# Optimization experiments

Measured on AMD Instinct MI355X. Metric: run time of the kernel, lower is better.

Reference implementation:

```python
import jax, jax.numpy as jnp
import numpy as np

D_EMBED = 64
N_HEADS = 4
D_HEAD = D_EMBED // N_HEADS
D_FF = 96          # int(1.5 * d_embed)
D_MODEL = 128      # repeat_factor = d_model // d_embed = 2
EPS = 1e-5
B = 4
# (idx_start, kernel_size, channels_in, kernel_no) per layer of the source CNN
LAYERS = [(0, 9, 8, 256), (18688, 9, 16, 256), (55808, 9, 16, 512)]
N_PARAMS = 130048
MAX_SEQ = max(ks * cin for _, ks, cin, _ in LAYERS) + 1  # 145


def _kernel_indices(start, ks, cin, kno):
    # Static ragged slice indices: per kernel, its weights plus trailing bias.
    L = ks * cin
    base = start + np.arange(kno)[:, None] * L + np.arange(L)[None, :]
    bias = start + kno * L + np.arange(kno)
    return np.concatenate([base, bias[:, None]], axis=1)  # (kno, L+1)


_IDX = [jnp.asarray(_kernel_indices(*l)) for l in LAYERS]


def setup_inputs():
    key = jax.random.key(0)
    k = jax.random.split(key, 8)
    s = 1.0 / np.sqrt(D_EMBED)
    return {
        "x": jax.random.normal(k[0], (B, N_PARAMS), dtype=jnp.float32),
        "pos_emb": jax.random.normal(k[1], (MAX_SEQ, D_EMBED), dtype=jnp.float32) * s,
        "comp_token": jax.random.normal(k[2], (D_EMBED,), dtype=jnp.float32),
        "in_proj_w": jax.random.normal(k[3], (3 * D_EMBED, D_EMBED), dtype=jnp.float32) * s,
        "in_proj_b": jnp.zeros((3 * D_EMBED,), jnp.float32),
        "out_proj_w": jax.random.normal(k[4], (D_EMBED, D_EMBED), dtype=jnp.float32) * s,
        "out_proj_b": jnp.zeros((D_EMBED,), jnp.float32),
        "lin1_w": jax.random.normal(k[5], (D_FF, D_EMBED), dtype=jnp.float32) * s,
        "lin1_b": jnp.zeros((D_FF,), jnp.float32),
        "lin2_w": jax.random.normal(k[6], (D_EMBED, D_FF), dtype=jnp.float32) / np.sqrt(D_FF),
        "lin2_b": jnp.zeros((D_EMBED,), jnp.float32),
        "ln1_w": jnp.ones((D_EMBED,), jnp.float32),
        "ln1_b": jnp.zeros((D_EMBED,), jnp.float32),
        "ln2_w": jnp.ones((D_EMBED,), jnp.float32),
        "ln2_b": jnp.zeros((D_EMBED,), jnp.float32),
    }


def _layernorm(x, w, b):
    mu = jnp.mean(x, axis=-1, keepdims=True)
    var = jnp.mean(jnp.square(x - mu), axis=-1, keepdims=True)
    return (x - mu) * jax.lax.rsqrt(var + EPS) * w + b


def _encoder(t, in_proj_w, in_proj_b, out_proj_w, out_proj_b,
             lin1_w, lin1_b, lin2_w, lin2_b, ln1_w, ln1_b, ln2_w, ln2_b):
    # Post-norm TransformerEncoderLayer (relu, eval mode -> dropout = identity).
    M, S, _ = t.shape
    qkv = t @ in_proj_w.T + in_proj_b                     # (M, S, 3D)
    q, k, v = jnp.split(qkv, 3, axis=-1)
    heads = lambda u: u.reshape(M, S, N_HEADS, D_HEAD).transpose(0, 2, 1, 3)
    q, k, v = heads(q), heads(k), heads(v)
    attn = jax.nn.softmax(jnp.einsum('mhsd,mhtd->mhst', q, k) / np.sqrt(D_HEAD))
    o = jnp.einsum('mhst,mhtd->mhsd', attn, v).transpose(0, 2, 1, 3).reshape(M, S, D_EMBED)
    o = o @ out_proj_w.T + out_proj_b
    h = _layernorm(t + o, ln1_w, ln1_b)
    ff = jax.nn.relu(h @ lin1_w.T + lin1_b) @ lin2_w.T + lin2_b
    return _layernorm(h + ff, ln2_w, ln2_b)


def reference(x, pos_emb, comp_token, in_proj_w, in_proj_b, out_proj_w, out_proj_b,
              lin1_w, lin1_b, lin2_w, lin2_b, ln1_w, ln1_b, ln2_w, ln2_b):
    enc = (in_proj_w, in_proj_b, out_proj_w, out_proj_b,
           lin1_w, lin1_b, lin2_w, lin2_b, ln1_w, ln1_b, ln2_w, ln2_b)
    outs = []
    for idx in _IDX:  # fixed small loop over layers; kernels within a layer are batched
        K, n = idx.shape
        w = x[:, idx]                                     # (B, K, n) ragged gather
        tok = w[..., None] + pos_emb[:n]                  # scalar -> d_embed broadcast + pos add
        cls = jnp.broadcast_to(comp_token, (B, K, 1, D_EMBED))
        tok = jnp.concatenate([cls, tok], axis=2).reshape(B * K, n + 1, D_EMBED)
        y = _encoder(tok, *enc)[:, 0, :]                  # comp-token readout
        outs.append(y.reshape(B, K, D_EMBED))
    y = jnp.concatenate(outs, axis=1)                     # (B, 1024, d_embed)
    return jnp.tile(y, (1, 1, D_MODEL // D_EMBED))        # (B, 1024, d_model)
```

## Files before the change

kernel.cpp:

```cpp
#include <hip/hip_runtime.h>
#include <math.h>

#define NPAR 130048
#define EPSF 1e-5f

typedef _Float16 hfp;
typedef _Float16 h2x __attribute__((ext_vector_type(2)));
typedef _Float16 h4x __attribute__((ext_vector_type(4)));
typedef float    f4x __attribute__((ext_vector_type(4)));

#define BSTR  164
#define VSTR2 172
#define ATSTR 172
#define WOSTR 76
#define L2STRH 108

#define L_W    0
#define L_WB   2304
#define L_ATT  2320
#define L_INVS 7824
#define L_O    7888
#define L_H1   8496
#define L_R    9104
#define L_PRE  9968
#define L_VPOS 11056
#define L_BETA 16560
#define L_QK   17216
#define L_SM   17344
#define SM_Q0   0
#define SM_KCLS 64
#define SM_VCLS 128
#define SM_UK   192
#define SM_UV   256
#define SM_ALPH 320
#define SM_GAM  324
#define SM_QB   328
#define LDS_FLOATS 17676

template<int C>
__device__ __forceinline__ float dppf(float x) {
    return __int_as_float(__builtin_amdgcn_update_dpp(0, __float_as_int(x), C, 0xf, 0xf, false));
}
__device__ __forceinline__ float rowsum16(float x) {
    x += dppf<0x128>(x); x += dppf<0x124>(x); x += dppf<0x122>(x); x += dppf<0x121>(x);
    return x;
}
__device__ __forceinline__ unsigned packh2(float a, float b) {
    union { h2x h; unsigned u; } cv;
    cv.h.x = (hfp)a; cv.h.y = (hfp)b;
    return cv.u;
}
__device__ __forceinline__ h4x cvt4(f4x v) {
    h4x r; r.x = (hfp)v.x; r.y = (hfp)v.y; r.z = (hfp)v.z; r.w = (hfp)v.w; return r;
}

template<int L>
__device__ __forceinline__ void run_group(
    const float* __restrict__ x,  const float* __restrict__ pe,
    const float* __restrict__ ct, const float* __restrict__ W,
    const float* __restrict__ bq, const float* __restrict__ Wo,
    const float* __restrict__ bo, const float* __restrict__ L1w,
    const float* __restrict__ b1, const float* __restrict__ L2w,
    const float* __restrict__ b2,
    const float* __restrict__ ln1w, const float* __restrict__ ln1b,
    const float* __restrict__ ln2w, const float* __restrict__ ln2b,
    float* __restrict__ lds, float* __restrict__ out,
    int b, int k0, int start, int kno, int kgo)
{
    const int tid  = threadIdx.x;
    const int wave = tid >> 6;
    const int lane = tid & 63;
    const int e16  = lane & 15;
    const int g4   = (lane >> 4) * 4;
    const int c0   = e16 * 4;
    const hfp* ldsh = (const hfp*)lds;

    {
        const f4x* src = (const f4x*)(x + (size_t)b*NPAR + start + (size_t)k0*L);
        f4x* dst = (f4x*)(lds + L_W);
        #pragma unroll
        for (int c = 0; c < (4*L + 255)/256; ++c) {
            int i4 = c*256 + tid;
            if (i4 < 4*L) dst[i4] = src[i4];
        }
        if (tid < 16) lds[L_WB + tid] = x[(size_t)b*NPAR + start + (size_t)kno*L + k0 + tid];
    }
    if (tid < 192) {
        const f4x* wr4 = (const f4x*)(W + tid*64);
        const f4x* ct4 = (const f4x*)ct;
        float dotc = bq[tid], rsum = 0.f;
        #pragma unroll
        for (int e = 0; e < 16; ++e) {
            f4x wv = wr4[e], cc = ct4[e];
            dotc += (wv.x*cc.x + wv.y*cc.y) + (wv.z*cc.z + wv.w*cc.w);
            rsum += (wv.x + wv.y) + (wv.z + wv.w);
        }
        const int cls = tid >> 6, o = tid & 63;
        if (cls == 0)      lds[L_SM + SM_Q0 + o] = dotc;
        else if (cls == 1) { lds[L_SM + SM_KCLS + o] = dotc; lds[L_SM + SM_UK + o] = rsum; }
        else               { lds[L_SM + SM_VCLS + o] = dotc; lds[L_SM + SM_UV + o] = rsum; }
    }

    h4x wof[4];
    #pragma unroll
    for (int kt = 0; kt < 4; ++kt)
        wof[kt] = cvt4(*(const f4x*)(Wo + (16*wave + e16)*64 + kt*16 + g4));
    h4x l1f[2][4];
    float b1v[2];
    #pragma unroll
    for (int u = 0; u < 2; ++u) {
        const int tt = wave + 4*u;
        if (tt < 6) {
            #pragma unroll
            for (int kt = 0; kt < 4; ++kt)
                l1f[u][kt] = cvt4(*(const f4x*)(L1w + (16*tt + e16)*64 + kt*16 + g4));
            b1v[u] = b1[16*tt + e16];
        }
    }
    h4x l2f[6];
    #pragma unroll
    for (int kt = 0; kt < 6; ++kt)
        l2f[kt] = cvt4(*(const f4x*)(L2w + (16*wave + e16)*96 + kt*16 + g4));
    const int nw = 16*wave + e16;
    const float boct = bo[nw] + ct[nw];
    const float b2v  = b2[nw];
    const f4x ln1w4 = *(const f4x*)(ln1w + c0);
    const f4x ln1b4 = *(const f4x*)(ln1b + c0);
    const f4x ln2w4 = *(const f4x*)(ln2w + c0);
    const f4x ln2b4 = *(const f4x*)(ln2b + c0);
    __syncthreads();

    {
        const int h = wave, d = lane;
        float acc = 0.f;
        #pragma unroll
        for (int e = 0; e < 16; ++e)
            acc += lds[L_SM + SM_Q0 + h*16 + e] * W[(64 + h*16 + e)*64 + d];
        ((hfp*)(lds + L_QK))[h*64 + d] = (hfp)acc;
    }
    if (lane < 16) {
        const int h = wave, e = lane;
        const float q0e = lds[L_SM + SM_Q0 + h*16 + e];
        float pa = q0e * lds[L_SM + SM_UK + h*16 + e];
        float pg = q0e * lds[L_SM + SM_KCLS + h*16 + e];
        float pq = q0e * bq[64 + h*16 + e];
        pa = rowsum16(pa); pg = rowsum16(pg); pq = rowsum16(pq);
        if (e == 0) {
            lds[L_SM + SM_ALPH + h] = pa;
            lds[L_SM + SM_GAM  + h] = pg;
            lds[L_SM + SM_QB   + h] = pq;
        }
    }
    __syncthreads();

    {
        const int w = wave, r16 = lane & 15, kg = lane >> 4;
        h4x av[4];
        #pragma unroll
        for (int kt = 0; kt < 4; ++kt)
            av[kt] = cvt4(*(const f4x*)(W + (128 + 16*w + r16)*64 + kt*16 + kg*4));
        h4x ab[4];
        #pragma unroll
        for (int kt = 0; kt < 4; ++kt) {
            if (r16 < 4) ab[kt] = *(const h4x*)((const hfp*)(lds + L_QK) + r16*64 + kt*16 + kg*4);
            else         { h4x z; z.x = (hfp)0.f; z.y = (hfp)0.f; z.z = (hfp)0.f; z.w = (hfp)0.f; ab[kt] = z; }
        }
        const f4x bv4 = *(const f4x*)(bq + 128 + 16*w + kg*4);
        hfp* vpos_h = (hfp*)(lds + L_VPOS);
        #pragma unroll
        for (int jt = 0; jt < 10; ++jt) {
            const int j = jt*16 + r16;
            h4x bf[4];
            #pragma unroll
            for (int kt = 0; kt < 4; ++kt) {
                if (j < 145) bf[kt] = cvt4(*(const f4x*)(pe + j*64 + kt*16 + kg*4));
                else { h4x z; z.x = (hfp)0.f; z.y = (hfp)0.f; z.z = (hfp)0.f; z.w = (hfp)0.f; bf[kt] = z; }
            }
            f4x acc = (f4x){0.f,0.f,0.f,0.f};
            #pragma unroll
            for (int kt = 0; kt < 4; ++kt)
                acc = __builtin_amdgcn_mfma_f32_16x16x16f16(av[kt], bf[kt], acc, 0, 0, 0);
            #pragma unroll
            for (int rr = 0; rr < 4; ++rr) {
                if (j < 145) vpos_h[(16*w + kg*4 + rr)*VSTR2 + j] = (hfp)(acc[rr] + bv4[rr]);
            }
            if ((jt & 3) == w) {
                f4x accb = (f4x){0.f,0.f,0.f,0.f};
                #pragma unroll
                for (int kt = 0; kt < 4; ++kt)
                    accb = __builtin_amdgcn_mfma_f32_16x16x16f16(ab[kt], bf[kt], accb, 0, 0, 0);
                if (lane < 16) {
                    const int jj = jt*16 + lane;
                    if (jj < 145) {
                        #pragma unroll
                        for (int rr = 0; rr < 4; ++rr)
                            lds[L_BETA + rr*BSTR + jj] = accb[rr] + lds[L_SM + SM_QB + rr];
                    }
                }
            }
        }
    }
    if (tid < 64) {
        hfp* vpos_h = (hfp*)(lds + L_VPOS);
        const int d = tid;
        #pragma unroll
        for (int c = 145; c < 156; ++c) vpos_h[d*VSTR2 + c] = (hfp)0.f;
        vpos_h[d*VSTR2 + 156] = (hfp)lds[L_SM + SM_VCLS + d];
        vpos_h[d*VSTR2 + 157] = (hfp)lds[L_SM + SM_UV + d];
        vpos_h[d*VSTR2 + 158] = (hfp)0.f;
        vpos_h[d*VSTR2 + 159] = (hfp)0.f;
    }
    __syncthreads();

    {
        const int r = tid >> 2;
        const int m = r >> 2, h = r & 3, q = tid & 3;
        const float alpha = lds[L_SM + SM_ALPH + h];
        const float gam   = lds[L_SM + SM_GAM  + h];
        const float* wr = lds + L_W + m*L;
        const float* br = lds + L_BETA + h*BSTR;
        const float wbias = lds[L_WB + m];

        float mx = 0.25f * gam;
        #pragma unroll
        for (int t = 0; t < 10; ++t) {
            const int j0 = 16*t + 4*q;
            if (j0 + 3 < L) {
                f4x wv = *(const f4x*)(wr + j0);
                f4x bv = *(const f4x*)(br + j0);
                mx = fmaxf(mx, fmaf(alpha, wv.x, bv.x)*0.25f);
                mx = fmaxf(mx, fmaf(alpha, wv.y, bv.y)*0.25f);
                mx = fmaxf(mx, fmaf(alpha, wv.z, bv.z)*0.25f);
                mx = fmaxf(mx, fmaf(alpha, wv.w, bv.w)*0.25f);
            } else if (j0 <= L) {
                #pragma unroll
                for (int ee = 0; ee < 4; ++ee) {
                    int j = j0 + ee;
                    if (j <= L) {
                        float w = (j < L) ? wr[j] : wbias;
                        mx = fmaxf(mx, fmaf(alpha, w, br[j])*0.25f);
                    }
                }
            }
        }
        mx = fmaxf(mx, __shfl_xor(mx, 1));
        mx = fmaxf(mx, __shfl_xor(mx, 2));
        const float M = mx;

        unsigned* arow32 = (unsigned*)(lds + L_ATT) + r*(ATSTR/2);
        float S = 0.f, WS = 0.f;
        #pragma unroll
        for (int t = 0; t < 10; ++t) {
            const int j0 = 16*t + 4*q;
            if (j0 + 3 < L) {
                f4x wv = *(const f4x*)(wr + j0);
                f4x bv = *(const f4x*)(br + j0);
                float p0 = __expf(fmaf(alpha, wv.x, bv.x)*0.25f - M);
                float p1 = __expf(fmaf(alpha, wv.y, bv.y)*0.25f - M);
                float p2 = __expf(fmaf(alpha, wv.z, bv.z)*0.25f - M);
                float p3 = __expf(fmaf(alpha, wv.w, bv.w)*0.25f - M);
                S  += (p0 + p1) + (p2 + p3);
                WS += (p0*wv.x + p1*wv.y) + (p2*wv.z + p3*wv.w);
                uint2 u; u.x = packh2(p0, p1); u.y = packh2(p2, p3);
                *(uint2*)(arow32 + (j0 >> 1)) = u;
            } else if (j0 <= L) {
                float pv4[4] = {0.f, 0.f, 0.f, 0.f};
                #pragma unroll
                for (int ee = 0; ee < 4; ++ee) {
                    int j = j0 + ee;
                    if (j <= L) {
                        float w = (j < L) ? wr[j] : wbias;
                        float p = __expf(fmaf(alpha, w, br[j])*0.25f - M);
                        S += p; WS += p*w; pv4[ee] = p;
                    }
                }
                uint2 u; u.x = packh2(pv4[0], pv4[1]); u.y = packh2(pv4[2], pv4[3]);
                *(uint2*)(arow32 + (j0 >> 1)) = u;
            } else if (j0 != 156) {
                uint2 z; z.x = 0u; z.y = 0u;
                *(uint2*)(arow32 + (j0 >> 1)) = z;
            }
        }
        S  += __shfl_xor(S, 1);  S  += __shfl_xor(S, 2);
        WS += __shfl_xor(WS, 1); WS += __shfl_xor(WS, 2);
        const float pc = __expf(0.25f*gam - M);
        S += pc;
        if (q == 0) {
            lds[L_INVS + r] = 1.f / S;
            arow32[78] = packh2(pc, WS);
            arow32[79] = 0u;
        }
    }
    __syncthreads();

    {
        const hfp* atth = ldsh + L_ATT*2;
        const hfp* vpos_h = ldsh + L_VPOS*2;
        const int hh = wave;
        f4x vacc = (f4x){0.f,0.f,0.f,0.f};
        #pragma unroll
        for (int kt = 0; kt < 10; ++kt) {
            h4x a  = *(const h4x*)(atth + (e16*4 + hh)*ATSTR + kt*16 + g4);
            h4x bf = *(const h4x*)(vpos_h + (16*hh + e16)*VSTR2 + kt*16 + g4);
            vacc = __builtin_amdgcn_mfma_f32_16x16x16f16(a, bf, vacc, 0, 0, 0);
        }
        hfp* Oh = (hfp*)(lds + L_O);
        #pragma unroll
        for (int rr = 0; rr < 4; ++rr) {
            float sc = lds[L_INVS + (g4 + rr)*4 + hh];
            Oh[(g4 + rr)*WOSTR + 16*hh + e16] = (hfp)(vacc[rr] * sc);
        }
    }
    __syncthreads();

    {
        const hfp* Oh = ldsh + L_O*2;
        f4x pacc = (f4x){0.f,0.f,0.f,0.f};
        #pragma unroll
        for (int kt = 0; kt < 4; ++kt) {
            h4x a = *(const h4x*)(Oh + e16*WOSTR + kt*16 + g4);
            pacc = __builtin_amdgcn_mfma_f32_16x16x16f16(a, wof[kt], pacc, 0, 0, 0);
        }
        #pragma unroll
        for (int rr = 0; rr < 4; ++rr)
            lds[L_PRE + (g4 + rr)*68 + nw] = pacc[rr] + boct;
    }
    __syncthreads();

    {
        const int m = wave*4 + (lane >> 4);
        f4x pv = *(const f4x*)(lds + L_PRE + m*68 + c0);
        float s = (pv.x + pv.y) + (pv.z + pv.w);
        float mu = rowsum16(s) * (1.f/64.f);
        f4x d; d.x = pv.x-mu; d.y = pv.y-mu; d.z = pv.z-mu; d.w = pv.w-mu;
        float v = (d.x*d.x + d.y*d.y) + (d.z*d.z + d.w*d.w);
        float rs = rsqrtf(rowsum16(v)*(1.f/64.f) + EPSF);
        h4x hv;
        hv.x = (hfp)(d.x*rs*ln1w4.x + ln1b4.x);
        hv.y = (hfp)(d.y*rs*ln1w4.y + ln1b4.y);
        hv.z = (hfp)(d.z*rs*ln1w4.z + ln1b4.z);
        hv.w = (hfp)(d.w*rs*ln1w4.w + ln1b4.w);
        *(h4x*)((hfp*)(lds + L_H1) + m*WOSTR + c0) = hv;
    }
    __syncthreads();

    {
        const hfp* H1h = ldsh + L_H1*2;
        h4x af[4];
        #pragma unroll
        for (int kt = 0; kt < 4; ++kt) af[kt] = *(const h4x*)(H1h + e16*WOSTR + kt*16 + g4);
        hfp* Rh = (hfp*)(lds + L_R);
        #pragma unroll
        for (int u = 0; u < 2; ++u) {
            const int tt = wave + 4*u;
            if (tt < 6) {
                f4x racc = (f4x){0.f,0.f,0.f,0.f};
                #pragma unroll
                for (int kt = 0; kt < 4; ++kt)
                    racc = __builtin_amdgcn_mfma_f32_16x16x16f16(af[kt], l1f[u][kt], racc, 0, 0, 0);
                const int n = 16*tt + e16;
                #pragma unroll
                for (int rr = 0; rr < 4; ++rr)
                    Rh[(g4 + rr)*L2STRH + n] = (hfp)fmaxf(racc[rr] + b1v[u], 0.f);
            }
        }
    }
    __syncthreads();

    {
        const hfp* Rh2 = ldsh + L_R*2;
        f4x yacc = (f4x){0.f,0.f,0.f,0.f};
        #pragma unroll
        for (int kt = 0; kt < 6; ++kt) {
            h4x a = *(const h4x*)(Rh2 + e16*L2STRH + kt*16 + g4);
            yacc = __builtin_amdgcn_mfma_f32_16x16x16f16(a, l2f[kt], yacc, 0, 0, 0);
        }
        #pragma unroll
        for (int rr = 0; rr < 4; ++rr)
            lds[L_PRE + (g4 + rr)*68 + nw] = yacc[rr] + b2v;
    }
    __syncthreads();

    {
        const int m = wave*4 + (lane >> 4);
        f4x pv = *(const f4x*)(lds + L_PRE + m*68 + c0);
        h4x h1p = *(const h4x*)((const hfp*)(lds + L_H1) + m*WOSTR + c0);
        f4x tot;
        tot.x = pv.x + (float)h1p.x;
        tot.y = pv.y + (float)h1p.y;
        tot.z = pv.z + (float)h1p.z;
        tot.w = pv.w + (float)h1p.w;
        float s = (tot.x + tot.y) + (tot.z + tot.w);
        float mu = rowsum16(s) * (1.f/64.f);
        f4x d; d.x = tot.x-mu; d.y = tot.y-mu; d.z = tot.z-mu; d.w = tot.w-mu;
        float v = (d.x*d.x + d.y*d.y) + (d.z*d.z + d.w*d.w);
        float rs = rsqrtf(rowsum16(v)*(1.f/64.f) + EPSF);
        f4x y;
        y.x = d.x*rs*ln2w4.x + ln2b4.x;
        y.y = d.y*rs*ln2w4.y + ln2b4.y;
        y.z = d.z*rs*ln2w4.z + ln2b4.z;
        y.w = d.w*rs*ln2w4.w + ln2b4.w;
        float* ob = out + ((size_t)b*1024 + kgo + k0 + m)*128;
        *(f4x*)(ob + c0)      = y;
        *(f4x*)(ob + 64 + c0) = y;
    }
}

__global__ __launch_bounds__(256, 1) void k_all(
    const float* __restrict__ x,  const float* __restrict__ pe,
    const float* __restrict__ ct, const float* __restrict__ W,
    const float* __restrict__ bq, const float* __restrict__ Wo,
    const float* __restrict__ bo, const float* __restrict__ L1w,
    const float* __restrict__ b1, const float* __restrict__ L2w,
    const float* __restrict__ b2,
    const float* __restrict__ ln1w, const float* __restrict__ ln1b,
    const float* __restrict__ ln2w, const float* __restrict__ ln2b,
    float* __restrict__ out)
{
    __shared__ __align__(16) float lds[LDS_FLOATS];
    const int w = blockIdx.x;
    if (w < 64) {
        run_group<72>(x, pe, ct, W, bq, Wo, bo, L1w, b1, L2w, b2,
                      ln1w, ln1b, ln2w, ln2b, lds, out,
                      w >> 4, (w & 15)*16, 0, 256, 0);
    } else if (w < 128) {
        const int g = w - 64;
        run_group<144>(x, pe, ct, W, bq, Wo, bo, L1w, b1, L2w, b2,
                       ln1w, ln1b, ln2w, ln2b, lds, out,
                       g >> 4, (g & 15)*16, 18688, 256, 256);
    } else {
        const int g = w - 128;
        run_group<144>(x, pe, ct, W, bq, Wo, bo, L1w, b1, L2w, b2,
                       ln1w, ln1b, ln2w, ln2b, lds, out,
                       g >> 5, (g & 31)*16, 55808, 512, 512);
    }
}

extern "C" void kernel_launch(void* const* d_in, const int* in_sizes, int n_in,
                              void* d_out, int out_size, void* d_ws, size_t ws_size,
                              hipStream_t stream) {
    const float* x    = (const float*)d_in[0];
    const float* pe   = (const float*)d_in[1];
    const float* ct   = (const float*)d_in[2];
    const float* Wq   = (const float*)d_in[3];
    const float* bq   = (const float*)d_in[4];
    const float* Wo   = (const float*)d_in[5];
    const float* bo   = (const float*)d_in[6];
    const float* L1w  = (const float*)d_in[7];
    const float* b1   = (const float*)d_in[8];
    const float* L2w  = (const float*)d_in[9];
    const float* b2   = (const float*)d_in[10];
    const float* ln1w = (const float*)d_in[11];
    const float* ln1b = (const float*)d_in[12];
    const float* ln2w = (const float*)d_in[13];
    const float* ln2b = (const float*)d_in[14];
    float* out = (float*)d_out;

    k_all<<<256, 256, 0, stream>>>(x, pe, ct, Wq, bq, Wo, bo, L1w, b1, L2w, b2,
                                   ln1w, ln1b, ln2w, ln2b, out);
}
```

Baseline: 19.26 us.

## Double block size to 512 threads, specializing extra waves for prologue and attention

Result: slower. 19.98 us (+3.7%).

```diff
diff --git a/kernel.cpp b/kernel.cpp
--- a/kernel.cpp
+++ b/kernel.cpp
@@ -53,6 +53,9 @@
 __device__ __forceinline__ h4x cvt4(f4x v) {
     h4x r; r.x = (hfp)v.x; r.y = (hfp)v.y; r.z = (hfp)v.z; r.w = (hfp)v.w; return r;
 }
+__device__ __forceinline__ h4x hzero() {
+    h4x z; z.x = (hfp)0.f; z.y = (hfp)0.f; z.z = (hfp)0.f; z.w = (hfp)0.f; return z;
+}
 
 template<int L>
 __device__ __forceinline__ void run_group(
@@ -75,85 +78,88 @@
     const int c0   = e16 * 4;
     const hfp* ldsh = (const hfp*)lds;
 
-    {
-        const f4x* src = (const f4x*)(x + (size_t)b*NPAR + start + (size_t)k0*L);
-        f4x* dst = (f4x*)(lds + L_W);
-        #pragma unroll
-        for (int c = 0; c < (4*L + 255)/256; ++c) {
-            int i4 = c*256 + tid;
-            if (i4 < 4*L) dst[i4] = src[i4];
-        }
-        if (tid < 16) lds[L_WB + tid] = x[(size_t)b*NPAR + start + (size_t)kno*L + k0 + tid];
-    }
-    if (tid < 192) {
-        const f4x* wr4 = (const f4x*)(W + tid*64);
-        const f4x* ct4 = (const f4x*)ct;
-        float dotc = bq[tid], rsum = 0.f;
-        #pragma unroll
-        for (int e = 0; e < 16; ++e) {
-            f4x wv = wr4[e], cc = ct4[e];
-            dotc += (wv.x*cc.x + wv.y*cc.y) + (wv.z*cc.z + wv.w*cc.w);
-            rsum += (wv.x + wv.y) + (wv.z + wv.w);
-        }
-        const int cls = tid >> 6, o = tid & 63;
-        if (cls == 0)      lds[L_SM + SM_Q0 + o] = dotc;
-        else if (cls == 1) { lds[L_SM + SM_KCLS + o] = dotc; lds[L_SM + SM_UK + o] = rsum; }
-        else               { lds[L_SM + SM_VCLS + o] = dotc; lds[L_SM + SM_UV + o] = rsum; }
-    }
-
-    h4x wof[4];
-    #pragma unroll
-    for (int kt = 0; kt < 4; ++kt)
-        wof[kt] = cvt4(*(const f4x*)(Wo + (16*wave + e16)*64 + kt*16 + g4));
-    h4x l1f[2][4];
-    float b1v[2];
-    #pragma unroll
-    for (int u = 0; u < 2; ++u) {
-        const int tt = wave + 4*u;
-        if (tt < 6) {
+    h4x wof[4], l1f[2][4], l2f[6];
+    float b1v[2], boct = 0.f, b2v = 0.f;
+    f4x ln1w4, ln1b4, ln2w4, ln2b4;
+    const int nw = 16*wave + e16;
+
+    if (wave < 4) {
+        {
+            const f4x* src = (const f4x*)(x + (size_t)b*NPAR + start + (size_t)k0*L);
+            f4x* dst = (f4x*)(lds + L_W);
             #pragma unroll
-            for (int kt = 0; kt < 4; ++kt)
-                l1f[u][kt] = cvt4(*(const f4x*)(L1w + (16*tt + e16)*64 + kt*16 + g4));
-            b1v[u] = b1[16*tt + e16];
-        }
-    }
-    h4x l2f[6];
-    #pragma unroll
-    for (int kt = 0; kt < 6; ++kt)
-        l2f[kt] = cvt4(*(const f4x*)(L2w + (16*wave + e16)*96 + kt*16 + g4));
-    const int nw = 16*wave + e16;
-    const float boct = bo[nw] + ct[nw];
-    const float b2v  = b2[nw];
-    const f4x ln1w4 = *(const f4x*)(ln1w + c0);
-    const f4x ln1b4 = *(const f4x*)(ln1b + c0);
-    const f4x ln2w4 = *(const f4x*)(ln2w + c0);
-    const f4x ln2b4 = *(const f4x*)(ln2b + c0);
-    __syncthreads();
-
-    {
+            for (int c = 0; c < (4*L + 255)/256; ++c) {
+                int i4 = c*256 + tid;
+                if (i4 < 4*L) dst[i4] = src[i4];
+            }
+            if (tid < 16) lds[L_WB + tid] = x[(size_t)b*NPAR + start + (size_t)kno*L + k0 + tid];
+        }
+        #pragma unroll
+        for (int kt = 0; kt < 4; ++kt)
+            wof[kt] = cvt4(*(const f4x*)(Wo + (16*wave + e16)*64 + kt*16 + g4));
+        #pragma unroll
+        for (int u = 0; u < 2; ++u) {
+            const int tt = wave + 4*u;
+            if (tt < 6) {
+                #pragma unroll
+                for (int kt = 0; kt < 4; ++kt)
+                    l1f[u][kt] = cvt4(*(const f4x*)(L1w + (16*tt + e16)*64 + kt*16 + g4));
+                b1v[u] = b1[16*tt + e16];
+            }
+        }
+        #pragma unroll
+        for (int kt = 0; kt < 6; ++kt)
+            l2f[kt] = cvt4(*(const f4x*)(L2w + (16*wave + e16)*96 + kt*16 + g4));
+        boct = bo[nw] + ct[nw];
+        b2v  = b2[nw];
+        ln1w4 = *(const f4x*)(ln1w + c0);
+        ln1b4 = *(const f4x*)(ln1b + c0);
+        ln2w4 = *(const f4x*)(ln2w + c0);
+        ln2b4 = *(const f4x*)(ln2b + c0);
+    } else {
+        const int t2 = tid - 256;
+        if (t2 < 192) {
+            const f4x* wr4 = (const f4x*)(W + t2*64);
+            const f4x* ct4 = (const f4x*)ct;
+            float dotc = bq[t2], rsum = 0.f;
+            #pragma unroll
+            for (int e = 0; e < 16; ++e) {
+                f4x wv = wr4[e], cc = ct4[e];
+                dotc += (wv.x*cc.x + wv.y*cc.y) + (wv.z*cc.z + wv.w*cc.w);
+                rsum += (wv.x + wv.y) + (wv.z + wv.w);
+            }
+            const int cls = t2 >> 6, o = t2 & 63;
+            if (cls == 0)      lds[L_SM + SM_Q0 + o] = dotc;
+            else if (cls == 1) { lds[L_SM + SM_KCLS + o] = dotc; lds[L_SM + SM_UK + o] = rsum; }
+            else               { lds[L_SM + SM_VCLS + o] = dotc; lds[L_SM + SM_UV + o] = rsum; }
+        }
+    }
+    __syncthreads();
+
+    if (wave < 4) {
         const int h = wave, d = lane;
         float acc = 0.f;
         #pragma unroll
         for (int e = 0; e < 16; ++e)
             acc += lds[L_SM + SM_Q0 + h*16 + e] * W[(64 + h*16 + e)*64 + d];
         ((hfp*)(lds + L_QK))[h*64 + d] = (hfp)acc;
-    }
-    if (lane < 16) {
-        const int h = wave, e = lane;
-        const float q0e = lds[L_SM + SM_Q0 + h*16 + e];
-        float pa = q0e * lds[L_SM + SM_UK + h*16 + e];
-        float pg = q0e * lds[L_SM + SM_KCLS + h*16 + e];
-        float pq = q0e * bq[64 + h*16 + e];
-        pa = rowsum16(pa); pg = rowsum16(pg); pq = rowsum16(pq);
-        if (e == 0) {
-            lds[L_SM + SM_ALPH + h] = pa;
-            lds[L_SM + SM_GAM  + h] = pg;
-            lds[L_SM + SM_QB   + h] = pq;
-        }
-    }
-    __syncthreads();
-
-    {
+        if (lane < 16) {
+            const int e = lane;
+            const float q0e = lds[L_SM + SM_Q0 + h*16 + e];
+            float pa = q0e * lds[L_SM + SM_UK + h*16 + e];
+            float pg = q0e * lds[L_SM + SM_KCLS + h*16 + e];
+            float pq = q0e * bq[64 + h*16 + e];
+            pa = rowsum16(pa); pg = rowsum16(pg); pq = rowsum16(pq);
+            if (e == 0) {
+                lds[L_SM + SM_ALPH + h] = pa;
+                lds[L_SM + SM_GAM  + h] = pg;
+                lds[L_SM + SM_QB   + h] = pq;
+            }
+        }
+    }
+    __syncthreads();
+
+    if (wave < 4) {
         const int w = wave, r16 = lane & 15, kg = lane >> 4;
         h4x av[4];
         #pragma unroll
@@ -163,7 +169,7 @@
         #pragma unroll
         for (int kt = 0; kt < 4; ++kt) {
             if (r16 < 4) ab[kt] = *(const h4x*)((const hfp*)(lds + L_QK) + r16*64 + kt*16 + kg*4);
-            else         { h4x z; z.x = (hfp)0.f; z.y = (hfp)0.f; z.z = (hfp)0.f; z.w = (hfp)0.f; ab[kt] = z; }
+            else         ab[kt] = hzero();
         }
         const f4x bv4 = *(const f4x*)(bq + 128 + 16*w + kg*4);
         hfp* vpos_h = (hfp*)(lds + L_VPOS);
@@ -172,10 +178,8 @@
             const int j = jt*16 + r16;
             h4x bf[4];
             #pragma unroll
-            for (int kt = 0; kt < 4; ++kt) {
-                if (j < 145) bf[kt] = cvt4(*(const f4x*)(pe + j*64 + kt*16 + kg*4));
-                else { h4x z; z.x = (hfp)0.f; z.y = (hfp)0.f; z.z = (hfp)0.f; z.w = (hfp)0.f; bf[kt] = z; }
-            }
+            for (int kt = 0; kt < 4; ++kt)
+                bf[kt] = (j < 145) ? cvt4(*(const f4x*)(pe + j*64 + kt*16 + kg*4)) : hzero();
             f4x acc = (f4x){0.f,0.f,0.f,0.f};
             #pragma unroll
             for (int kt = 0; kt < 4; ++kt)
@@ -213,8 +217,8 @@
     __syncthreads();
 
     {
-        const int r = tid >> 2;
-        const int m = r >> 2, h = r & 3, q = tid & 3;
+        const int r = tid >> 3;
+        const int m = r >> 2, h = r & 3, q = tid & 7;
         const float alpha = lds[L_SM + SM_ALPH + h];
         const float gam   = lds[L_SM + SM_GAM  + h];
         const float* wr = lds + L_W + m*L;
@@ -223,8 +227,8 @@
 
         float mx = 0.25f * gam;
         #pragma unroll
-        for (int t = 0; t < 10; ++t) {
-            const int j0 = 16*t + 4*q;
+        for (int t = 0; t < 5; ++t) {
+            const int j0 = 32*t + 4*q;
             if (j0 + 3 < L) {
                 f4x wv = *(const f4x*)(wr + j0);
                 f4x bv = *(const f4x*)(br + j0);
@@ -245,13 +249,14 @@
         }
         mx = fmaxf(mx, __shfl_xor(mx, 1));
         mx = fmaxf(mx, __shfl_xor(mx, 2));
+        mx = fmaxf(mx, __shfl_xor(mx, 4));
         const float M = mx;
 
         unsigned* arow32 = (unsigned*)(lds + L_ATT) + r*(ATSTR/2);
         float S = 0.f, WS = 0.f;
         #pragma unroll
-        for (int t = 0; t < 10; ++t) {
-            const int j0 = 16*t + 4*q;
+        for (int t = 0; t < 5; ++t) {
+            const int j0 = 32*t + 4*q;
             if (j0 + 3 < L) {
                 f4x wv = *(const f4x*)(wr + j0);
                 f4x bv = *(const f4x*)(br + j0);
@@ -281,8 +286,8 @@
                 *(uint2*)(arow32 + (j0 >> 1)) = z;
             }
         }
-        S  += __shfl_xor(S, 1);  S  += __shfl_xor(S, 2);
-        WS += __shfl_xor(WS, 1); WS += __shfl_xor(WS, 2);
+        S  += __shfl_xor(S, 1);  S  += __shfl_xor(S, 2);  S  += __shfl_xor(S, 4);
+        WS += __shfl_xor(WS, 1); WS += __shfl_xor(WS, 2); WS += __shfl_xor(WS, 4);
         const float pc = __expf(0.25f*gam - M);
         S += pc;
         if (q == 0) {
@@ -293,7 +298,7 @@
     }
     __syncthreads();
 
-    {
+    if (wave < 4) {
         const hfp* atth = ldsh + L_ATT*2;
         const hfp* vpos_h = ldsh + L_VPOS*2;
         const int hh = wave;
@@ -313,7 +318,7 @@
     }
     __syncthreads();
 
-    {
+    if (wave < 4) {
         const hfp* Oh = ldsh + L_O*2;
         f4x pacc = (f4x){0.f,0.f,0.f,0.f};
         #pragma unroll
@@ -327,7 +332,7 @@
     }
     __syncthreads();
 
-    {
+    if (wave < 4) {
         const int m = wave*4 + (lane >> 4);
         f4x pv = *(const f4x*)(lds + L_PRE + m*68 + c0);
         float s = (pv.x + pv.y) + (pv.z + pv.w);
@@ -344,7 +349,7 @@
     }
     __syncthreads();
 
-    {
+    if (wave < 4) {
         const hfp* H1h = ldsh + L_H1*2;
         h4x af[4];
         #pragma unroll
@@ -367,7 +372,7 @@
     }
     __syncthreads();
 
-    {
+    if (wave < 4) {
         const hfp* Rh2 = ldsh + L_R*2;
         f4x yacc = (f4x){0.f,0.f,0.f,0.f};
         #pragma unroll
@@ -381,7 +386,7 @@
     }
     __syncthreads();
 
-    {
+    if (wave < 4) {
         const int m = wave*4 + (lane >> 4);
         f4x pv = *(const f4x*)(lds + L_PRE + m*68 + c0);
         h4x h1p = *(const h4x*)((const hfp*)(lds + L_H1) + m*WOSTR + c0);
@@ -406,7 +411,7 @@
     }
 }
 
-__global__ __launch_bounds__(256, 1) void k_all(
+__global__ __launch_bounds__(512, 1) void k_all(
     const float* __restrict__ x,  const float* __restrict__ pe,
     const float* __restrict__ ct, const float* __restrict__ W,
     const float* __restrict__ bq, const float* __restrict__ Wo,
@@ -456,6 +461,6 @@
     const float* ln2b = (const float*)d_in[14];
     float* out = (float*)d_out;
 
-    k_all<<<256, 256, 0, stream>>>(x, pe, ct, Wq, bq, Wo, bo, L1w, b1, L2w, b2,
+    k_all<<<256, 512, 0, stream>>>(x, pe, ct, Wq, bq, Wo, bo, L1w, b1, L2w, b2,
                                    ln1w, ln1b, ln2w, ln2b, out);
 }
```
